# Optimization experiments

Measured on AMD Instinct MI355X. Metric: run time of the kernel, lower is better.

The kernel has to match this reference:

```python
import jax, jax.numpy as jnp
import numpy as np

H = 50  # hidden size fixed by the module


def setup_inputs() -> dict:
    key = jax.random.key(0)
    ks = jax.random.split(key, 7)
    B, T = 2048, 512
    s = 1.0 / np.sqrt(H)  # PyTorch default uniform(-1/sqrt(H), 1/sqrt(H)) scale, approximated with scaled normals
    return {
        "x": jax.random.normal(ks[0], (B, T, 1), dtype=jnp.float32),
        "W_ih": jax.random.normal(ks[1], (4 * H, 1), dtype=jnp.float32) * s,
        "W_hh": jax.random.normal(ks[2], (4 * H, H), dtype=jnp.float32) * s,
        "b_ih": jax.random.normal(ks[3], (4 * H,), dtype=jnp.float32) * s,
        "b_hh": jax.random.normal(ks[4], (4 * H,), dtype=jnp.float32) * s,
        "W_lin": jax.random.normal(ks[5], (1, H), dtype=jnp.float32) * s,
        "b_lin": jax.random.normal(ks[6], (1,), dtype=jnp.float32) * s,
    }


def reference(x, W_ih, W_hh, b_ih, b_hh, W_lin, b_lin):
    B, T, _ = x.shape
    # Precompute input projection for all timesteps: [B, T, 4H]
    xproj = jnp.einsum('bti,gi->btg', x, W_ih) + b_ih + b_hh
    xproj_t = jnp.transpose(xproj, (1, 0, 2))  # [T, B, 4H] for scan over time

    h0 = jnp.zeros((B, H), dtype=x.dtype)
    c0 = jnp.zeros((B, H), dtype=x.dtype)

    def step(carry, xt):
        h, c = carry
        gates = xt + h @ W_hh.T  # [B, 4H]
        i, f, g, o = jnp.split(gates, 4, axis=-1)  # PyTorch gate order i,f,g,o
        i = jax.nn.sigmoid(i)
        f = jax.nn.sigmoid(f)
        g = jnp.tanh(g)
        o = jax.nn.sigmoid(o)
        c = f * c + i * g
        h = o * jnp.tanh(c)
        return (h, c), None

    (h_last, _), _ = jax.lax.scan(step, (h0, c0), xproj_t)
    # x[:, -1, :] of LSTM output == final hidden state h_T
    return h_last @ W_lin.T + b_lin  # [B, 1]
```

## Files before the change

### kernel.cpp

```cpp
#include <hip/hip_runtime.h>

#define HSZ 50
#define TSZ 512
#define NB  4
#define KPAD 72

typedef _Float16 half8  __attribute__((ext_vector_type(8)));
typedef float   floatx4 __attribute__((ext_vector_type(4)));

__device__ __forceinline__ float sig_y(float y) {
    return __builtin_amdgcn_rcpf(1.0f + __builtin_amdgcn_exp2f(y));
}
__device__ __forceinline__ float tanh_y(float y) {
    return fmaf(-2.0f, __builtin_amdgcn_rcpf(1.0f + __builtin_amdgcn_exp2f(y)), 1.0f);
}

__global__ __launch_bounds__(256)
void lstm_mir4(const float* __restrict__ x,
               const float* __restrict__ W_ih,
               const float* __restrict__ W_hh,
               const float* __restrict__ b_ih,
               const float* __restrict__ b_hh,
               const float* __restrict__ W_lin,
               const float* __restrict__ b_lin,
               float* __restrict__ out)
{
    __shared__ float xs[TSZ][NB];
    __shared__ __align__(16) _Float16 hlds[2][16][KPAD];

    const int tid = threadIdx.x;
    const int w   = tid >> 6;
    const int ln  = tid & 63;
    const int n   = ln & 15;
    const int q   = ln >> 4;
    const int rr  = n >> 2;
    const int bb  = n & 3;
    const int b0  = blockIdx.x * NB;

    const float* xg = x + (size_t)b0 * TSZ;
    for (int i = tid; i < NB * TSZ; i += 256)
        xs[i & (TSZ - 1)][i >> 9] = xg[i];
    for (int i = tid; i < 2 * 16 * KPAD; i += 256)
        ((_Float16*)hlds)[i] = (i % KPAD == 50) ? (_Float16)1.0f : (_Float16)0.0f;

    const int uA = 16 * w + n;
    half8 af[4][2];
#pragma unroll
    for (int g = 0; g < 4; ++g) {
        const float gs = (g == 2) ? 2.88539008f : -1.44269504f;
        const int row = g * HSZ + uA;
        const bool rok = (uA < HSZ);
#pragma unroll
        for (int kt = 0; kt < 2; ++kt) {
#pragma unroll
            for (int j = 0; j < 8; ++j) {
                const int k = kt * 32 + q * 8 + j;
                float v = 0.0f;
                if (rok) {
                    if (k < HSZ)      v = W_hh[row * HSZ + k];
                    else if (k == 50) v = b_ih[row] + b_hh[row];
                    else if (k == 51) v = W_ih[row];
                }
                af[g][kt][j] = (_Float16)(v * gs);
            }
        }
    }

    float c0 = 0.0f;
    __syncthreads();
    if (tid < 16)
        hlds[0][tid][51] = (_Float16)xs[0][tid & 3];
    __syncthreads();

    const floatx4 zero4 = {0.0f, 0.0f, 0.0f, 0.0f};
    const int u = 16 * w + 4 * q + rr;
    _Float16* const hwp0 = &hlds[0][bb][u];
    _Float16* const hwp1 = &hlds[1][bb][u];
    const bool xl50 = (w == 3) && (q == 0) && (rr == 2);
    const bool xl51 = (w == 3) && (q == 0) && (rr == 3);

#pragma unroll 2
    for (int t = 0; t < TSZ; ++t) {
        const int rb = t & 1, wb = rb ^ 1;

        const half8 bf0 = *(const half8*)&hlds[rb][n][q * 8];
        const half8 bf1 = *(const half8*)&hlds[rb][n][32 + q * 8];

        float xnext = 0.0f;
        if (w == 3) xnext = xs[(t + 1) & (TSZ - 1)][ln & 3];

        floatx4 acc[4];
#pragma unroll
        for (int g = 0; g < 4; ++g) {
            acc[g] = __builtin_amdgcn_mfma_f32_16x16x32_f16(af[g][0], bf0, zero4,  0, 0, 0);
            acc[g] = __builtin_amdgcn_mfma_f32_16x16x32_f16(af[g][1], bf1, acc[g], 0, 0, 0);
        }

        float pre[4];
#pragma unroll
        for (int g = 0; g < 4; ++g) {
            const float v01 = (rr & 1) ? acc[g][1] : acc[g][0];
            const float v23 = (rr & 1) ? acc[g][3] : acc[g][2];
            pre[g] = (rr & 2) ? v23 : v01;
        }

        const float i0 = sig_y (pre[0]);
        const float f0 = sig_y (pre[1]);
        const float g0 = tanh_y(pre[2]);
        const float o0 = sig_y (pre[3]);
        c0 = fmaf(f0, c0, i0 * g0);
        float h0 = o0 * tanh_y(c0 * 2.88539008f);
        if (xl50) h0 = 1.0f;
        if (xl51) h0 = xnext;

        const _Float16 hh = (_Float16)h0;
        _Float16* const hw = wb ? hwp1 : hwp0;
        hw[0]         = hh;
        hw[4  * KPAD] = hh;
        hw[8  * KPAD] = hh;
        hw[12 * KPAD] = hh;
        __syncthreads();
    }

    if (w == 0 && ln < NB) {
        float acc = b_lin[0];
        for (int uu = 0; uu < HSZ; ++uu)
            acc = fmaf((float)hlds[0][ln][uu], W_lin[uu], acc);
        out[(size_t)b0 + ln] = acc;
    }
}

extern "C" void kernel_launch(void* const* d_in, const int* in_sizes, int n_in,
                              void* d_out, int out_size, void* d_ws, size_t ws_size,
                              hipStream_t stream) {
    const float* x     = (const float*)d_in[0];
    const float* W_ih  = (const float*)d_in[1];
    const float* W_hh  = (const float*)d_in[2];
    const float* b_ih  = (const float*)d_in[3];
    const float* b_hh  = (const float*)d_in[4];
    const float* W_lin = (const float*)d_in[5];
    const float* b_lin = (const float*)d_in[6];
    float* outp = (float*)d_out;

    const int B = in_sizes[0] / TSZ;
    hipLaunchKernelGGL(lstm_mir4, dim3(B / NB), dim3(256), 0, stream,
                       x, W_ih, W_hh, b_ih, b_hh, W_lin, b_lin, outp);
}
```

Before: 262.3 us.

## Run each LSTM block as a single wavefront, interleaving gates in MFMA rows

Moves the per-block recurrence from four wavefronts to one 64-lane wavefront. That wavefront holds all 13 weight tiles in registers, with gates interleaved so each lane gets i,f,g,o for its unit in one accumulator. The per-step __syncthreads is replaced by an LDS waitcnt, which removes cross-wave barrier cost and the fourfold replicated h writes. In exchange each wave does 26 MFMAs and four cell updates serially per step, and register pressure rises sharply.

```diff
diff --git a/kernel.cpp b/kernel.cpp
--- a/kernel.cpp
+++ b/kernel.cpp
@@ -3,7 +3,7 @@
 #define HSZ 50
 #define TSZ 512
 #define NB  4
-#define KPAD 72
+#define KPAD 96
 
 typedef _Float16 half8  __attribute__((ext_vector_type(8)));
 typedef float   floatx4 __attribute__((ext_vector_type(4)));
@@ -15,118 +15,123 @@
     return fmaf(-2.0f, __builtin_amdgcn_rcpf(1.0f + __builtin_amdgcn_exp2f(y)), 1.0f);
 }
 
-__global__ __launch_bounds__(256)
-void lstm_mir4(const float* __restrict__ x,
-               const float* __restrict__ W_ih,
-               const float* __restrict__ W_hh,
-               const float* __restrict__ b_ih,
-               const float* __restrict__ b_hh,
-               const float* __restrict__ W_lin,
-               const float* __restrict__ b_lin,
-               float* __restrict__ out)
+__global__ __launch_bounds__(64, 1)
+void lstm_1w(const float* __restrict__ x,
+             const float* __restrict__ W_ih,
+             const float* __restrict__ W_hh,
+             const float* __restrict__ b_ih,
+             const float* __restrict__ b_hh,
+             const float* __restrict__ W_lin,
+             const float* __restrict__ b_lin,
+             float* __restrict__ out)
 {
     __shared__ float xs[TSZ][NB];
-    __shared__ __align__(16) _Float16 hlds[2][16][KPAD];
+    __shared__ __align__(16) _Float16 hlds[2][NB][KPAD];
 
-    const int tid = threadIdx.x;
-    const int w   = tid >> 6;
-    const int ln  = tid & 63;
-    const int n   = ln & 15;
-    const int q   = ln >> 4;
-    const int rr  = n >> 2;
-    const int bb  = n & 3;
-    const int b0  = blockIdx.x * NB;
+    const int ln = threadIdx.x;
+    const int n  = ln & 15;
+    const int q  = ln >> 4;
+    const int rr = n >> 2;
+    const int b  = n & 3;
+    const int b0 = blockIdx.x * NB;
 
     const float* xg = x + (size_t)b0 * TSZ;
-    for (int i = tid; i < NB * TSZ; i += 256)
+    for (int i = ln; i < NB * TSZ; i += 64)
         xs[i & (TSZ - 1)][i >> 9] = xg[i];
-    for (int i = tid; i < 2 * 16 * KPAD; i += 256)
+    for (int i = ln; i < 2 * NB * KPAD; i += 64)
         ((_Float16*)hlds)[i] = (i % KPAD == 50) ? (_Float16)1.0f : (_Float16)0.0f;
 
-    const int uA = 16 * w + n;
-    half8 af[4][2];
+    half8 af[13][2];
+    {
+        const int g  = n & 3;
+        const int ub = n >> 2;
+        const float gs = (g == 2) ? 2.88539008f : -1.44269504f;
 #pragma unroll
-    for (int g = 0; g < 4; ++g) {
-        const float gs = (g == 2) ? 2.88539008f : -1.44269504f;
-        const int row = g * HSZ + uA;
-        const bool rok = (uA < HSZ);
+        for (int j = 0; j < 13; ++j) {
+            const int u = 4 * j + ub;
+            const int wrow = g * HSZ + u;
+            const bool ok = (u < HSZ);
 #pragma unroll
-        for (int kt = 0; kt < 2; ++kt) {
+            for (int kt = 0; kt < 2; ++kt) {
 #pragma unroll
-            for (int j = 0; j < 8; ++j) {
-                const int k = kt * 32 + q * 8 + j;
-                float v = 0.0f;
-                if (rok) {
-                    if (k < HSZ)      v = W_hh[row * HSZ + k];
-                    else if (k == 50) v = b_ih[row] + b_hh[row];
-                    else if (k == 51) v = W_ih[row];
+                for (int jj = 0; jj < 8; ++jj) {
+                    const int k = kt * 32 + q * 8 + jj;
+                    float v = 0.0f;
+                    if (ok) {
+                        if (k < HSZ)      v = W_hh[wrow * HSZ + k];
+                        else if (k == 50) v = b_ih[wrow] + b_hh[wrow];
+                        else if (k == 51) v = W_ih[wrow];
+                    }
+                    af[j][kt][jj] = (_Float16)(v * gs);
                 }
-                af[g][kt][j] = (_Float16)(v * gs);
             }
         }
     }
 
-    float c0 = 0.0f;
+    float c0 = 0.0f, c1 = 0.0f, c2 = 0.0f, c3 = 0.0f;
     __syncthreads();
-    if (tid < 16)
-        hlds[0][tid][51] = (_Float16)xs[0][tid & 3];
+    if (ln < NB) hlds[0][ln][51] = (_Float16)xs[0][ln];
     __syncthreads();
 
     const floatx4 zero4 = {0.0f, 0.0f, 0.0f, 0.0f};
-    const int u = 16 * w + 4 * q + rr;
-    _Float16* const hwp0 = &hlds[0][bb][u];
-    _Float16* const hwp1 = &hlds[1][bb][u];
-    const bool xl50 = (w == 3) && (q == 0) && (rr == 2);
-    const bool xl51 = (w == 3) && (q == 0) && (rr == 3);
 
 #pragma unroll 2
     for (int t = 0; t < TSZ; ++t) {
         const int rb = t & 1, wb = rb ^ 1;
 
-        const half8 bf0 = *(const half8*)&hlds[rb][n][q * 8];
-        const half8 bf1 = *(const half8*)&hlds[rb][n][32 + q * 8];
+        const half8 bf0 = *(const half8*)&hlds[rb][b][q * 8];
+        const half8 bf1 = *(const half8*)&hlds[rb][b][32 + q * 8];
+        const float xnext = xs[(t + 1) & (TSZ - 1)][b];
 
-        float xnext = 0.0f;
-        if (w == 3) xnext = xs[(t + 1) & (TSZ - 1)][ln & 3];
-
-        floatx4 acc[4];
+        floatx4 acc[13];
 #pragma unroll
-        for (int g = 0; g < 4; ++g) {
-            acc[g] = __builtin_amdgcn_mfma_f32_16x16x32_f16(af[g][0], bf0, zero4,  0, 0, 0);
-            acc[g] = __builtin_amdgcn_mfma_f32_16x16x32_f16(af[g][1], bf1, acc[g], 0, 0, 0);
+        for (int j = 0; j < 13; ++j) {
+            acc[j] = __builtin_amdgcn_mfma_f32_16x16x32_f16(af[j][0], bf0, zero4,  0, 0, 0);
+            acc[j] = __builtin_amdgcn_mfma_f32_16x16x32_f16(af[j][1], bf1, acc[j], 0, 0, 0);
         }
 
-        float pre[4];
-#pragma unroll
-        for (int g = 0; g < 4; ++g) {
-            const float v01 = (rr & 1) ? acc[g][1] : acc[g][0];
-            const float v23 = (rr & 1) ? acc[g][3] : acc[g][2];
-            pre[g] = (rr & 2) ? v23 : v01;
+        _Float16* const hw = &hlds[wb][b][0];
+
+#define CELL_M(MI, CV)                                                         \
+        {                                                                      \
+            const floatx4 t0 = (rr & 1) ? acc[4*MI+1] : acc[4*MI+0];           \
+            const floatx4 t1 = (rr & 1) ? acc[4*MI+3] : acc[4*MI+2];           \
+            const floatx4 pr = (rr & 2) ? t1 : t0;                             \
+            const float i_ = sig_y (pr[0]);                                    \
+            const float f_ = sig_y (pr[1]);                                    \
+            const float g_ = tanh_y(pr[2]);                                    \
+            const float o_ = sig_y (pr[3]);                                    \
+            CV = fmaf(f_, CV, i_ * g_);                                        \
+            const float h_ = o_ * tanh_y(CV * 2.88539008f);                    \
+            hw[16 * MI + 4 * rr + q] = (_Float16)h_;                           \
+        }
+        CELL_M(0, c0)
+        CELL_M(1, c1)
+        CELL_M(2, c2)
+#undef CELL_M
+
+        {
+            const floatx4 pr = acc[12];
+            const float i_ = sig_y (pr[0]);
+            const float f_ = sig_y (pr[1]);
+            const float g_ = tanh_y(pr[2]);
+            const float o_ = sig_y (pr[3]);
+            c3 = fmaf(f_, c3, i_ * g_);
+            const float h_ = o_ * tanh_y(c3 * 2.88539008f);
+            if (rr == 0) {
+                if (q < 2)  hw[48 + q] = (_Float16)h_;
+                if (q == 3) hw[51] = (_Float16)xnext;
+            }
         }
 
-        const float i0 = sig_y (pre[0]);
-        const float f0 = sig_y (pre[1]);
-        const float g0 = tanh_y(pre[2]);
-        const float o0 = sig_y (pre[3]);
-        c0 = fmaf(f0, c0, i0 * g0);
-        float h0 = o0 * tanh_y(c0 * 2.88539008f);
-        if (xl50) h0 = 1.0f;
-        if (xl51) h0 = xnext;
-
-        const _Float16 hh = (_Float16)h0;
-        _Float16* const hw = wb ? hwp1 : hwp0;
-        hw[0]         = hh;
-        hw[4  * KPAD] = hh;
-        hw[8  * KPAD] = hh;
-        hw[12 * KPAD] = hh;
-        __syncthreads();
+        asm volatile("s_waitcnt lgkmcnt(0)" ::: "memory");
     }
 
-    if (w == 0 && ln < NB) {
-        float acc = b_lin[0];
-        for (int uu = 0; uu < HSZ; ++uu)
-            acc = fmaf((float)hlds[0][ln][uu], W_lin[uu], acc);
-        out[(size_t)b0 + ln] = acc;
+    if (ln < NB) {
+        float accv = b_lin[0];
+        for (int u = 0; u < HSZ; ++u)
+            accv = fmaf((float)hlds[0][ln][u], W_lin[u], accv);
+        out[(size_t)b0 + ln] = accv;
     }
 }
 
@@ -143,6 +148,6 @@
     float* outp = (float*)d_out;
 
     const int B = in_sizes[0] / TSZ;
-    hipLaunchKernelGGL(lstm_mir4, dim3(B / NB), dim3(256), 0, stream,
+    hipLaunchKernelGGL(lstm_1w, dim3(B / NB), dim3(64), 0, stream,
                        x, W_ih, W_hh, b_ih, b_hh, W_lin, b_lin, outp);
 }
```

Result: slower. 410.0 us (+56.3%).
